# Optimization experiments

Measured on AMD Instinct MI355X. Metric: run time of the kernel, lower is better.

## Reference

```python
import jax, jax.numpy as jnp
import numpy as np

EPS = 1e-06
SINKHORN_ITERS = 3


def _sinkhorn_knopp(P, iters=SINKHORN_ITERS, eps=EPS):
    # P: [n, n] positive matrix -> approximately doubly stochastic
    for _ in range(iters):
        P = P / (P.sum(axis=-1, keepdims=True) + eps)
        P = P / (P.sum(axis=-2, keepdims=True) + eps)
    return P


def setup_inputs() -> dict:
    key = jax.random.key(0)
    k1, k2, k3, k4 = jax.random.split(key, 4)
    B, n, C = 8192, 4, 2048
    x = jax.random.normal(k1, (B, n, C), dtype=jnp.float32)
    rmsnorm_weight = jnp.ones((C,), dtype=jnp.float32)
    H_pre = jax.random.normal(k2, (n,), dtype=jnp.float32)
    H_post = jax.random.normal(k3, (n,), dtype=jnp.float32)
    H_res = jax.random.normal(k4, (n, n), dtype=jnp.float32)
    return {"x": x, "rmsnorm_weight": rmsnorm_weight, "H_pre": H_pre,
            "H_post": H_post, "H_res": H_res}


def reference(x, rmsnorm_weight, H_pre, H_post, H_res):
    # x: [B, n, C] float32
    # 1) sigmoid-weighted stream aggregation: [B, C]
    H_pre_act = jax.nn.sigmoid(H_pre)
    x_agg = jnp.einsum('bnc,n->bc', x, H_pre_act)
    # 2) RMSNorm in bf16 (rms computed in fp32, matching torch fallback)
    x_agg_bf16 = x_agg.astype(jnp.bfloat16)
    rms = jnp.sqrt(jnp.mean(x_agg_bf16.astype(jnp.float32) ** 2, axis=-1,
                            keepdims=True) + EPS)  # [B, 1] fp32
    w_bf16 = rmsnorm_weight.astype(jnp.bfloat16)
    y_norm = x_agg_bf16 / rms * w_bf16[None, :]  # promoted to fp32 by rms
    # 3) Sinkhorn-Knopp on exp(H_res): [n, n]
    M = _sinkhorn_knopp(jnp.exp(H_res))
    # 4) mix streams and combine
    H_post_act = 2.0 * jax.nn.sigmoid(H_post)
    mixed = jnp.einsum('ij,bjc->bic', M, x)  # [B, n, C]
    out = mixed + H_post_act[None, :, None] * y_norm.astype(jnp.float32)[:, None, :]
    return out
```

## Files before the change

### kernel.cpp

```cpp
#include <hip/hip_runtime.h>
#include <hip/hip_bf16.h>


namespace {

constexpr int N = 4;
constexpr int C = 2048;
constexpr int BLOCK = 256;
constexpr int CPT = C / BLOCK;
constexpr int VEC = CPT / 4;
constexpr float EPSF = 1e-6f;

__device__ __forceinline__ float bf16r(float v) {
    return __bfloat162float(__float2bfloat16(v));
}

__global__ __launch_bounds__(BLOCK) void mhc_kernel(
    const float* __restrict__ x,
    const float* __restrict__ w,
    const float* __restrict__ H_pre,
    const float* __restrict__ H_post,
    const float* __restrict__ H_res,
    float* __restrict__ out)
{
    const int b = blockIdx.x;
    const int t = threadIdx.x;

    __shared__ float s_pre[N];
    __shared__ float s_post[N];
    __shared__ float s_P[N][N];
    __shared__ float s_red[BLOCK / 64];
    __shared__ float s_rinv;

    if (t == 0) {
        float P[N][N];
        #pragma unroll
        for (int j = 0; j < N; ++j) {
            s_pre[j]  = 1.0f / (1.0f + expf(-H_pre[j]));
            s_post[j] = 2.0f / (1.0f + expf(-H_post[j]));
        }
        #pragma unroll
        for (int i = 0; i < N; ++i)
            #pragma unroll
            for (int j = 0; j < N; ++j)
                P[i][j] = expf(H_res[i * N + j]);
        #pragma unroll
        for (int it = 0; it < 3; ++it) {
            #pragma unroll
            for (int i = 0; i < N; ++i) {
                float rs = P[i][0] + P[i][1] + P[i][2] + P[i][3] + EPSF;
                #pragma unroll
                for (int j = 0; j < N; ++j) P[i][j] = P[i][j] / rs;
            }
            #pragma unroll
            for (int j = 0; j < N; ++j) {
                float cs = P[0][j] + P[1][j] + P[2][j] + P[3][j] + EPSF;
                #pragma unroll
                for (int i = 0; i < N; ++i) P[i][j] = P[i][j] / cs;
            }
        }
        #pragma unroll
        for (int i = 0; i < N; ++i)
            #pragma unroll
            for (int j = 0; j < N; ++j)
                s_P[i][j] = P[i][j];
    }

    const size_t base = (size_t)b * N * C;
    float xs[N][CPT];
    float ws[CPT];
    #pragma unroll
    for (int j = 0; j < N; ++j) {
        #pragma unroll
        for (int v = 0; v < VEC; ++v) {
            const float4 tmp =
                *(const float4*)(x + base + (size_t)j * C + (size_t)(v * BLOCK + t) * 4);
            xs[j][v * 4 + 0] = tmp.x;
            xs[j][v * 4 + 1] = tmp.y;
            xs[j][v * 4 + 2] = tmp.z;
            xs[j][v * 4 + 3] = tmp.w;
        }
    }
    #pragma unroll
    for (int v = 0; v < VEC; ++v) {
        const float4 tmp = *(const float4*)(w + (size_t)(v * BLOCK + t) * 4);
        ws[v * 4 + 0] = bf16r(tmp.x);
        ws[v * 4 + 1] = bf16r(tmp.y);
        ws[v * 4 + 2] = bf16r(tmp.z);
        ws[v * 4 + 3] = bf16r(tmp.w);
    }

    __syncthreads();

    const float p0 = s_pre[0], p1 = s_pre[1], p2 = s_pre[2], p3 = s_pre[3];

    float agg[CPT];
    float ss = 0.0f;
    #pragma unroll
    for (int k = 0; k < CPT; ++k) {
        float a = p0 * xs[0][k] + p1 * xs[1][k] + p2 * xs[2][k] + p3 * xs[3][k];
        a = bf16r(a);
        agg[k] = a;
        ss += a * a;
    }

    #pragma unroll
    for (int off = 32; off > 0; off >>= 1) ss += __shfl_down(ss, off, 64);
    if ((t & 63) == 0) s_red[t >> 6] = ss;
    __syncthreads();
    if (t == 0) {
        float tot = 0.0f;
        #pragma unroll
        for (int i = 0; i < BLOCK / 64; ++i) tot += s_red[i];
        s_rinv = 1.0f / sqrtf(tot / (float)C + EPSF);
    }
    __syncthreads();
    const float rinv = s_rinv;

    float M[N][N], post[N];
    #pragma unroll
    for (int i = 0; i < N; ++i) {
        post[i] = s_post[i];
        #pragma unroll
        for (int j = 0; j < N; ++j) M[i][j] = s_P[i][j];
    }

    #pragma unroll
    for (int i = 0; i < N; ++i) {
        #pragma unroll
        for (int v = 0; v < VEC; ++v) {
            float o[4];
            #pragma unroll
            for (int k = 0; k < 4; ++k) {
                const int idx = v * 4 + k;
                const float yn = agg[idx] * rinv * ws[idx];
                o[k] = M[i][0] * xs[0][idx] + M[i][1] * xs[1][idx]
                     + M[i][2] * xs[2][idx] + M[i][3] * xs[3][idx]
                     + post[i] * yn;
            }
            *(float4*)(out + base + (size_t)i * C + (size_t)(v * BLOCK + t) * 4) =
                *(const float4*)o;
        }
    }
}

}

extern "C" void kernel_launch(void* const* d_in, const int* in_sizes, int n_in,
                              void* d_out, int out_size, void* d_ws, size_t ws_size,
                              hipStream_t stream) {
    const float* x      = (const float*)d_in[0];
    const float* w      = (const float*)d_in[1];
    const float* H_pre  = (const float*)d_in[2];
    const float* H_post = (const float*)d_in[3];
    const float* H_res  = (const float*)d_in[4];
    float* out = (float*)d_out;

    const int B = in_sizes[0] / (N * C);
    mhc_kernel<<<dim3(B), dim3(BLOCK), 0, stream>>>(x, w, H_pre, H_post, H_res, out);
}
```

Measured before the change: 436.8 us.

## Hoist Sinkhorn setup into separate kernel and use nontemporal loads/stores

Moves the per-block sigmoid and Sinkhorn computation into a one-thread setup kernel that writes constants to workspace, which the main kernel reads directly. This removes the serial thread-0 prologue and one of the block barriers. It also switches x loads and output stores to nontemporal builtins and has every thread compute the final reduction instead of broadcasting it through shared memory. The cost is an extra kernel launch and dependence on the workspace buffer.

```diff
diff --git a/kernel.cpp b/kernel.cpp
--- a/kernel.cpp
+++ b/kernel.cpp
@@ -11,125 +11,118 @@
 constexpr int VEC = CPT / 4;
 constexpr float EPSF = 1e-6f;
 
+typedef float f4 __attribute__((ext_vector_type(4)));
+
 __device__ __forceinline__ float bf16r(float v) {
     return __bfloat162float(__float2bfloat16(v));
+}
+
+__global__ void setup_kernel(const float* __restrict__ H_pre,
+                             const float* __restrict__ H_post,
+                             const float* __restrict__ H_res,
+                             float* __restrict__ cst) {
+    if (threadIdx.x != 0 || blockIdx.x != 0) return;
+    float P[N][N];
+    #pragma unroll
+    for (int j = 0; j < N; ++j) {
+        cst[j]     = 1.0f / (1.0f + expf(-H_pre[j]));
+        cst[N + j] = 2.0f / (1.0f + expf(-H_post[j]));
+    }
+    #pragma unroll
+    for (int i = 0; i < N; ++i)
+        #pragma unroll
+        for (int j = 0; j < N; ++j)
+            P[i][j] = expf(H_res[i * N + j]);
+    #pragma unroll
+    for (int it = 0; it < 3; ++it) {
+        #pragma unroll
+        for (int i = 0; i < N; ++i) {
+            float rs = P[i][0] + P[i][1] + P[i][2] + P[i][3] + EPSF;
+            #pragma unroll
+            for (int j = 0; j < N; ++j) P[i][j] /= rs;
+        }
+        #pragma unroll
+        for (int j = 0; j < N; ++j) {
+            float cs = P[0][j] + P[1][j] + P[2][j] + P[3][j] + EPSF;
+            #pragma unroll
+            for (int i = 0; i < N; ++i) P[i][j] /= cs;
+        }
+    }
+    #pragma unroll
+    for (int i = 0; i < N; ++i)
+        #pragma unroll
+        for (int j = 0; j < N; ++j)
+            cst[2 * N + i * N + j] = P[i][j];
 }
 
 __global__ __launch_bounds__(BLOCK) void mhc_kernel(
     const float* __restrict__ x,
     const float* __restrict__ w,
-    const float* __restrict__ H_pre,
-    const float* __restrict__ H_post,
-    const float* __restrict__ H_res,
+    const float* __restrict__ cst,
     float* __restrict__ out)
 {
     const int b = blockIdx.x;
     const int t = threadIdx.x;
 
-    __shared__ float s_pre[N];
-    __shared__ float s_post[N];
-    __shared__ float s_P[N][N];
     __shared__ float s_red[BLOCK / 64];
-    __shared__ float s_rinv;
 
-    if (t == 0) {
-        float P[N][N];
+    float pre[N], post[N], M[N][N];
+    #pragma unroll
+    for (int j = 0; j < N; ++j) {
+        pre[j]  = cst[j];
+        post[j] = cst[N + j];
+    }
+    #pragma unroll
+    for (int i = 0; i < N; ++i)
         #pragma unroll
-        for (int j = 0; j < N; ++j) {
-            s_pre[j]  = 1.0f / (1.0f + expf(-H_pre[j]));
-            s_post[j] = 2.0f / (1.0f + expf(-H_post[j]));
-        }
-        #pragma unroll
-        for (int i = 0; i < N; ++i)
-            #pragma unroll
-            for (int j = 0; j < N; ++j)
-                P[i][j] = expf(H_res[i * N + j]);
-        #pragma unroll
-        for (int it = 0; it < 3; ++it) {
-            #pragma unroll
-            for (int i = 0; i < N; ++i) {
-                float rs = P[i][0] + P[i][1] + P[i][2] + P[i][3] + EPSF;
-                #pragma unroll
-                for (int j = 0; j < N; ++j) P[i][j] = P[i][j] / rs;
-            }
-            #pragma unroll
-            for (int j = 0; j < N; ++j) {
-                float cs = P[0][j] + P[1][j] + P[2][j] + P[3][j] + EPSF;
-                #pragma unroll
-                for (int i = 0; i < N; ++i) P[i][j] = P[i][j] / cs;
-            }
-        }
-        #pragma unroll
-        for (int i = 0; i < N; ++i)
-            #pragma unroll
-            for (int j = 0; j < N; ++j)
-                s_P[i][j] = P[i][j];
-    }
+        for (int j = 0; j < N; ++j)
+            M[i][j] = cst[2 * N + i * N + j];
 
     const size_t base = (size_t)b * N * C;
     float xs[N][CPT];
-    float ws[CPT];
     #pragma unroll
     for (int j = 0; j < N; ++j) {
         #pragma unroll
         for (int v = 0; v < VEC; ++v) {
-            const float4 tmp =
-                *(const float4*)(x + base + (size_t)j * C + (size_t)(v * BLOCK + t) * 4);
-            xs[j][v * 4 + 0] = tmp.x;
-            xs[j][v * 4 + 1] = tmp.y;
-            xs[j][v * 4 + 2] = tmp.z;
-            xs[j][v * 4 + 3] = tmp.w;
+            const f4 tmp = __builtin_nontemporal_load(
+                (const f4*)(x + base + (size_t)j * C + (size_t)(v * BLOCK + t) * 4));
+            #pragma unroll
+            for (int k = 0; k < 4; ++k) xs[j][v * 4 + k] = tmp[k];
         }
     }
+    float ws[CPT];
     #pragma unroll
     for (int v = 0; v < VEC; ++v) {
-        const float4 tmp = *(const float4*)(w + (size_t)(v * BLOCK + t) * 4);
-        ws[v * 4 + 0] = bf16r(tmp.x);
-        ws[v * 4 + 1] = bf16r(tmp.y);
-        ws[v * 4 + 2] = bf16r(tmp.z);
-        ws[v * 4 + 3] = bf16r(tmp.w);
+        const f4 tmp = *(const f4*)(w + (size_t)(v * BLOCK + t) * 4);
+        #pragma unroll
+        for (int k = 0; k < 4; ++k) ws[v * 4 + k] = bf16r(tmp[k]);
     }
-
-    __syncthreads();
-
-    const float p0 = s_pre[0], p1 = s_pre[1], p2 = s_pre[2], p3 = s_pre[3];
 
     float agg[CPT];
     float ss = 0.0f;
     #pragma unroll
     for (int k = 0; k < CPT; ++k) {
-        float a = p0 * xs[0][k] + p1 * xs[1][k] + p2 * xs[2][k] + p3 * xs[3][k];
+        float a = pre[0] * xs[0][k] + pre[1] * xs[1][k]
+                + pre[2] * xs[2][k] + pre[3] * xs[3][k];
         a = bf16r(a);
         agg[k] = a;
         ss += a * a;
     }
 
     #pragma unroll
-    for (int off = 32; off > 0; off >>= 1) ss += __shfl_down(ss, off, 64);
+    for (int off = 32; off > 0; off >>= 1) ss += __shfl_xor(ss, off, 64);
     if ((t & 63) == 0) s_red[t >> 6] = ss;
     __syncthreads();
-    if (t == 0) {
-        float tot = 0.0f;
-        #pragma unroll
-        for (int i = 0; i < BLOCK / 64; ++i) tot += s_red[i];
-        s_rinv = 1.0f / sqrtf(tot / (float)C + EPSF);
-    }
-    __syncthreads();
-    const float rinv = s_rinv;
-
-    float M[N][N], post[N];
+    float tot = 0.0f;
     #pragma unroll
-    for (int i = 0; i < N; ++i) {
-        post[i] = s_post[i];
-        #pragma unroll
-        for (int j = 0; j < N; ++j) M[i][j] = s_P[i][j];
-    }
+    for (int i = 0; i < BLOCK / 64; ++i) tot += s_red[i];
+    const float rinv = 1.0f / sqrtf(tot * (1.0f / (float)C) + EPSF);
 
     #pragma unroll
     for (int i = 0; i < N; ++i) {
         #pragma unroll
         for (int v = 0; v < VEC; ++v) {
-            float o[4];
+            f4 o;
             #pragma unroll
             for (int k = 0; k < 4; ++k) {
                 const int idx = v * 4 + k;
@@ -138,8 +131,8 @@
                      + M[i][2] * xs[2][idx] + M[i][3] * xs[3][idx]
                      + post[i] * yn;
             }
-            *(float4*)(out + base + (size_t)i * C + (size_t)(v * BLOCK + t) * 4) =
-                *(const float4*)o;
+            __builtin_nontemporal_store(
+                o, (f4*)(out + base + (size_t)i * C + (size_t)(v * BLOCK + t) * 4));
         }
     }
 }
@@ -155,7 +148,10 @@
     const float* H_post = (const float*)d_in[3];
     const float* H_res  = (const float*)d_in[4];
     float* out = (float*)d_out;
+    float* cst = (float*)d_ws;
 
     const int B = in_sizes[0] / (N * C);
-    mhc_kernel<<<dim3(B), dim3(BLOCK), 0, stream>>>(x, w, H_pre, H_post, H_res, out);
+
+    setup_kernel<<<dim3(1), dim3(1), 0, stream>>>(H_pre, H_post, H_res, cst);
+    mhc_kernel<<<dim3(B), dim3(BLOCK), 0, stream>>>(x, w, cst, out);
 }
```

After: 424.2 us. 2.9% less time.
